# Kernel optimization log

Hardware: AMD Instinct MI355X
Metric: run time of the kernel (lower is better)

## Reference

```python
import jax, jax.numpy as jnp
import numpy as np

B, S1, S2 = 8, 2048, 2048
K1_DIM = K2_DIM = 512
PK1_DIM = PK2_DIM = 256
ATT_DIM = 512
DV = 512


def setup_inputs() -> dict:
    key = jax.random.key(0)
    ks = jax.random.split(key, 16)
    s = 0.02
    inp = {
        "k1": jax.random.normal(ks[0], (B, S1, K1_DIM), jnp.float32),
        "k2": jax.random.normal(ks[1], (B, S2, K2_DIM), jnp.float32),
        "preserved_k1": jax.random.normal(ks[2], (B, S1, PK1_DIM), jnp.float32),
        "preserved_k2": jax.random.normal(ks[3], (B, S2, PK2_DIM), jnp.float32),
        "v1": jax.random.normal(ks[4], (B, S1, DV), jnp.float32),
        "v2": jax.random.normal(ks[5], (B, S2, DV), jnp.float32),
        # Linear params stored as [in, out] (x @ W + b == torch Linear)
        "W_k1": jax.random.normal(ks[6], (K1_DIM, ATT_DIM), jnp.float32) * s,
        "b_k1": jnp.zeros((ATT_DIM,), jnp.float32),
        "W_k2": jax.random.normal(ks[7], (K2_DIM, ATT_DIM), jnp.float32) * s,
        "b_k2": jnp.zeros((ATT_DIM,), jnp.float32),
        "W_pk1": jax.random.normal(ks[8], (K1_DIM + PK1_DIM, ATT_DIM), jnp.float32) * s,
        "b_pk1": jnp.zeros((ATT_DIM,), jnp.float32),
        "W_pk2": jax.random.normal(ks[9], (K2_DIM + PK2_DIM, ATT_DIM), jnp.float32) * s,
        "b_pk2": jnp.zeros((ATT_DIM,), jnp.float32),
        # lengths in [S/2, S) so no softmax row is fully masked (original exits on NaN)
        "k1_lengths": jax.random.randint(ks[10], (B,), S1 // 2, S1, jnp.int32).astype(jnp.int64),
        "k2_lengths": jax.random.randint(ks[11], (B,), S2 // 2, S2, jnp.int32).astype(jnp.int64),
    }
    return inp


def _mask(k1_lengths, k2_lengths):
    # Faithful to the original loop: a position is masked iff EXACTLY ONE of
    # (row >= l1) / (col >= l2) holds (mask counter == 1, not >= 1).
    row_over = (jnp.arange(S1)[None, :, None] >= k1_lengths[:, None, None])  # [B,S1,1]
    col_over = (jnp.arange(S2)[None, None, :] >= k2_lengths[:, None, None])  # [B,1,S2]
    return (row_over.astype(jnp.int32) + col_over.astype(jnp.int32)) == 1  # [B,S1,S2]


def reference(k1, k2, preserved_k1, preserved_k2, v1, v2,
              W_k1, b_k1, W_k2, b_k2, W_pk1, b_pk1, W_pk2, b_pk2,
              k1_lengths, k2_lengths):
    pk1 = jnp.concatenate([k1, preserved_k1], axis=-1) @ W_pk1 + b_pk1  # [B,S1,A]
    pk2 = jnp.concatenate([k2, preserved_k2], axis=-1) @ W_pk2 + b_pk2  # [B,S2,A]
    k1p = k1 @ W_k1 + b_k1  # [B,S1,A]
    k2p = k2 @ W_k2 + b_k2  # [B,S2,A]

    score_1 = jnp.einsum("bsa,bta->bst", k1p, pk2)   # [B,S1,S2]
    score_2 = jnp.einsum("bsa,bta->bst", pk1, k2p)   # [B,S1,S2]

    mask = _mask(k1_lengths, k2_lengths)
    score_1 = jnp.where(mask, -jnp.inf, score_1)
    score_2 = jnp.where(mask, -jnp.inf, score_2)

    w1 = jax.nn.softmax(jnp.swapaxes(score_1, 1, 2), axis=-1)  # [B,S2,S1]
    w2 = jax.nn.softmax(score_2, axis=-1)                      # [B,S1,S2]

    o1 = jnp.einsum("bts,bsd->btd", w1, v1)  # [B,S2,DV]
    o2 = jnp.einsum("bst,btd->bsd", w2, v2)  # [B,S1,DV]
    # NOTE: original returns ragged per-sample slices of w1/w2; we return the
    # full padded weight matrices (slice w1[i,:l2,:l1], w2[i,:l1,:l2] to match).
    return (o1, o2, w1, w2)
```

## Files before the change

kernel.cpp:

```cpp
#include <hip/hip_runtime.h>

typedef _Float16 half8 __attribute__((ext_vector_type(8)));
typedef float    floatx4 __attribute__((ext_vector_type(4)));
typedef unsigned short u16;

constexpr int Bn  = 8;
constexpr int Sq  = 2048;
constexpr int KD  = 512;
constexpr int PKD = 256;
constexpr int AD  = 512;
constexpr int DV  = 512;

__device__ __forceinline__ void llds16(const void* g, void* l)
{
    __builtin_amdgcn_global_load_lds(
        (const __attribute__((address_space(1))) unsigned int*)g,
        (__attribute__((address_space(3))) unsigned int*)l, 16, 0, 0);
}

__global__ __launch_bounds__(256)
void transpose_cast_k(const float* __restrict__ in0, const float* __restrict__ in1,
                      _Float16* __restrict__ out0, _Float16* __restrict__ out1,
                      int inRows, int inCols, long long bsIn, long long bsOut,
                      int zsplit)
{
    __shared__ float t[32][33];
    const int bz = blockIdx.z;
    const bool sel = (bz >= zsplit);
    const int b = sel ? bz - zsplit : bz;
    const float* in = (sel ? in1 : in0) + (long long)b * bsIn;
    _Float16* out = (sel ? out1 : out0) + (long long)b * bsOut;
    const int tx = threadIdx.x & 31;
    const int ty = threadIdx.x >> 5;
    const int c0 = blockIdx.x * 32;
    const int r0 = blockIdx.y * 32;
#pragma unroll
    for (int i = 0; i < 4; ++i)
        t[ty + 8*i][tx] = in[(long long)(r0 + ty + 8*i) * inCols + c0 + tx];
    __syncthreads();
#pragma unroll
    for (int i = 0; i < 4; ++i)
        out[(long long)(c0 + ty + 8*i) * inRows + r0 + tx] = (_Float16)t[tx][ty + 8*i];
}

__global__ __launch_bounds__(256)
void wT_all_k(const float* __restrict__ Wk1, const float* __restrict__ Wk2,
              const float* __restrict__ Wpk1, const float* __restrict__ Wpk2,
              _Float16* __restrict__ Tk1, _Float16* __restrict__ Tk2,
              _Float16* __restrict__ Tpk1, _Float16* __restrict__ Tpk2)
{
    const int z = blockIdx.z;
    const float* W; _Float16* T; int Krows;
    if      (z == 0) { W = Wk1;  T = Tk1;  Krows = KD; }
    else if (z == 1) { W = Wk2;  T = Tk2;  Krows = KD; }
    else if (z == 2) { W = Wpk1; T = Tpk1; Krows = KD + PKD; }
    else             { W = Wpk2; T = Tpk2; Krows = KD + PKD; }
    const int r0 = blockIdx.y * 32;
    if (r0 >= Krows) return;
    const int c0 = blockIdx.x * 32;
    __shared__ float t[32][33];
    const int tx = threadIdx.x & 31;
    const int ty = threadIdx.x >> 5;
#pragma unroll
    for (int i = 0; i < 4; ++i)
        t[ty + 8*i][tx] = W[(long long)(r0 + ty + 8*i) * AD + c0 + tx];
    __syncthreads();
#pragma unroll
    for (int i = 0; i < 4; ++i)
        T[(long long)(c0 + ty + 8*i) * Krows + r0 + tx] = (_Float16)t[tx][ty + 8*i];
}

__global__ __launch_bounds__(256)
void cast_cat_k(const float* __restrict__ x0, const float* __restrict__ y0,
                _Float16* __restrict__ o0,
                const float* __restrict__ x1, const float* __restrict__ y1,
                _Float16* __restrict__ o1)
{
    const bool sel = (blockIdx.z != 0);
    const float* x = sel ? x1 : x0;
    const float* y = sel ? y1 : y0;
    _Float16* out = sel ? o1 : o0;
    const int idx = blockIdx.x * 256 + threadIdx.x;
    const int e   = idx * 8;
    const int r   = e / 768;
    const int c   = e % 768;
    const float* src = (c < 512) ? (x + (long long)r * 512 + c)
                                 : (y + (long long)r * 256 + (c - 512));
    const floatx4 f0 = *(const floatx4*)(src);
    const floatx4 f1 = *(const floatx4*)(src + 4);
    half8 h;
#pragma unroll
    for (int j = 0; j < 4; ++j) { h[j] = (_Float16)f0[j]; h[4 + j] = (_Float16)f1[j]; }
    *(half8*)(out + (long long)e) = h;
}

template<bool A_F32, bool OUT_F16>
__global__ __launch_bounds__(256, 2)
void gemm_k(const void* __restrict__ A1v, const void* __restrict__ A2v, int Ksplit,
            int lda1, int lda2, long long bsA,
            const _Float16* __restrict__ Bm, int ldb, long long bsB,
            void* __restrict__ Cv, int ldc, long long bsC,
            const float* __restrict__ bias, int K)
{
    __shared__ __align__(16) unsigned char AsRaw[A_F32 ? 16384 : 8192];
    __shared__ __align__(16) unsigned char BsRaw[8192];

    const int tid  = threadIdx.x;
    const int lane = tid & 63;
    const int wave = tid >> 6;
    const int wm   = (wave >> 1) * 64;
    const int wn   = (wave & 1) * 64;
    const int fr   = lane & 15;
    const int fq   = lane >> 4;

    const int tm = blockIdx.y, tn = blockIdx.x, bz = blockIdx.z;
    const long long aRowBase = (long long)tm * 128;
    const long long bRowBase = (long long)tn * 128;
    const _Float16* Bbase = Bm + (long long)bz * bsB;

    floatx4 acc[4][4];
#pragma unroll
    for (int i = 0; i < 4; ++i)
#pragma unroll
        for (int j = 0; j < 4; ++j) acc[i][j] = (floatx4)0.0f;

    for (int k0 = 0; k0 < K; k0 += 32) {
        __syncthreads();

        if (A_F32) {
            const float* A1 = (const float*)A1v + (long long)bz * bsA;
            const float* A2 = (const float*)A2v;
#pragma unroll
            for (int is = 0; is < 4; ++is) {
                const int r  = (tid >> 3) + is * 32;
                const int ch = (tid & 7) ^ (r & 7);
                const int kk = k0 + ch * 4;
                const float* src = (kk < Ksplit)
                    ? A1 + (aRowBase + r) * lda1 + kk
                    : A2 + (aRowBase + r) * lda2 + (kk - Ksplit);
                llds16(src, AsRaw + tid * 16 + is * 4096);
            }
        } else {
            const _Float16* A1 = (const _Float16*)A1v + (long long)bz * bsA;
#pragma unroll
            for (int is = 0; is < 2; ++is) {
                const int r  = (tid >> 2) + is * 64;
                const int ch = (tid & 3) ^ (r & 3);
                llds16(A1 + (aRowBase + r) * lda1 + k0 + ch * 8,
                       AsRaw + tid * 16 + is * 4096);
            }
        }
#pragma unroll
        for (int is = 0; is < 2; ++is) {
            const int r  = (tid >> 2) + is * 64;
            const int ch = (tid & 3) ^ (r & 3);
            llds16(Bbase + (bRowBase + r) * ldb + k0 + ch * 8,
                   BsRaw + tid * 16 + is * 4096);
        }

        __syncthreads();

        half8 af[4], bf[4];
        if (A_F32) {
            const float* As32 = (const float*)AsRaw;
#pragma unroll
            for (int i = 0; i < 4; ++i) {
                const int r  = wm + i * 16 + fr;
                const int c0 = ((2 * fq) ^ (r & 7)) * 4;
                const int c1 = ((2 * fq + 1) ^ (r & 7)) * 4;
                floatx4 f0 = *(const floatx4*)(As32 + r * 32 + c0);
                floatx4 f1 = *(const floatx4*)(As32 + r * 32 + c1);
                half8 h;
#pragma unroll
                for (int j = 0; j < 4; ++j) {
                    h[j]     = (_Float16)f0[j];
                    h[4 + j] = (_Float16)f1[j];
                }
                af[i] = h;
            }
        } else {
            const _Float16* As16 = (const _Float16*)AsRaw;
#pragma unroll
            for (int i = 0; i < 4; ++i) {
                const int r  = wm + i * 16 + fr;
                const int ch = fq ^ (r & 3);
                af[i] = *(const half8*)(As16 + r * 32 + ch * 8);
            }
        }
        {
            const _Float16* Bs16 = (const _Float16*)BsRaw;
#pragma unroll
            for (int j = 0; j < 4; ++j) {
                const int r  = wn + j * 16 + fr;
                const int ch = fq ^ (r & 3);
                bf[j] = *(const half8*)(Bs16 + r * 32 + ch * 8);
            }
        }
#pragma unroll
        for (int i = 0; i < 4; ++i)
#pragma unroll
            for (int j = 0; j < 4; ++j)
                acc[i][j] = __builtin_amdgcn_mfma_f32_16x16x32_f16(af[i], bf[j], acc[i][j], 0, 0, 0);
    }

    const int crow0 = tm * 128 + wm + fq * 4;
    const int ccol0 = tn * 128 + wn + fr;
    if (OUT_F16) {
        _Float16* C = (_Float16*)Cv + (long long)bz * bsC;
#pragma unroll
        for (int i = 0; i < 4; ++i)
#pragma unroll
            for (int j = 0; j < 4; ++j) {
                const int col = ccol0 + j * 16;
                const float bv = bias[col];
#pragma unroll
                for (int r = 0; r < 4; ++r)
                    C[(long long)(crow0 + i*16 + r) * ldc + col] = (_Float16)(acc[i][j][r] + bv);
            }
    } else {
        float* C = (float*)Cv + (long long)bz * bsC;
#pragma unroll
        for (int i = 0; i < 4; ++i)
#pragma unroll
            for (int j = 0; j < 4; ++j) {
                const int col = ccol0 + j * 16;
#pragma unroll
                for (int r = 0; r < 4; ++r)
                    C[(long long)(crow0 + i*16 + r) * ldc + col] = acc[i][j][r];
            }
    }
}

template<bool OUT16>
__global__ __launch_bounds__(512, 2)
void gemm256_k(const _Float16* __restrict__ A0, const _Float16* __restrict__ A1,
               const _Float16* __restrict__ B0, const _Float16* __restrict__ B1,
               void* __restrict__ C0v, void* __restrict__ C1v,
               long long bsA, int lda, long long bsB, int ldb,
               long long bsC, int ldc, int K, int zsplit)
{
    __shared__ __align__(16) _Float16 lds[65536];

    const int nwg  = 64 * gridDim.z;
    const int lin0 = (blockIdx.z * 8 + blockIdx.y) * 8 + blockIdx.x;
    const int cpx  = nwg >> 3;
    const int lin  = (lin0 & 7) * cpx + (lin0 >> 3);
    const int tn   = lin & 7;
    const int tm   = (lin >> 3) & 7;
    const int bz   = lin >> 6;

    const bool sel = (bz >= zsplit);
    const int  bzl = sel ? (bz - zsplit) : bz;
    const _Float16* Am = sel ? A1 : A0;
    const _Float16* Bm = sel ? B1 : B0;

    const int tid  = threadIdx.x;
    const int lane = tid & 63;
    const int wave = tid >> 6;
    const int wm   = (wave >> 2) * 128;
    const int wn   = (wave & 3) * 64;
    const int fr   = lane & 15;
    const int fq   = lane >> 4;

    const _Float16* Ab = Am + (long long)bzl * bsA + (long long)tm * 256 * lda;
    const _Float16* Bb = Bm + (long long)bzl * bsB + (long long)tn * 256 * ldb;

    const int sr = lane >> 3;
    const int ch = (lane & 7) ^ sr;
    const _Float16* srcA[2][2];
    const _Float16* srcB[2][2];
#pragma unroll
    for (int h = 0; h < 2; ++h)
#pragma unroll
        for (int l = 0; l < 2; ++l) {
            const int r = h * 128 + (wave * 2 + l) * 8 + sr;
            srcA[h][l] = Ab + (long long)r * lda + ch * 8;
            srcB[h][l] = Bb + (long long)r * ldb + ch * 8;
        }

    auto stageA = [&](int kt, int buf) {
#pragma unroll
        for (int h = 0; h < 2; ++h)
#pragma unroll
            for (int l = 0; l < 2; ++l)
                llds16(srcA[h][l] + kt * 64,
                       lds + buf * 32768 + h * 8192 + (wave * 2 + l) * 512 + lane * 8);
    };
    auto stageB = [&](int kt, int buf) {
#pragma unroll
        for (int h = 0; h < 2; ++h)
#pragma unroll
            for (int l = 0; l < 2; ++l)
                llds16(srcB[h][l] + kt * 64,
                       lds + buf * 32768 + 16384 + h * 8192 + (wave * 2 + l) * 512 + lane * 8);
    };

    auto rdA = [&](int buf, int im, int kk) -> half8 {
        const int row = wm + im * 16 + fr;
        const int c   = (kk * 4 + fq) ^ (row & 7);
        return *(const half8*)(lds + buf * 32768 + row * 64 + c * 8);
    };
    auto rdB = [&](int buf, int jn, int kk) -> half8 {
        const int row = wn + jn * 16 + fr;
        const int c   = (kk * 4 + fq) ^ (row & 7);
        return *(const half8*)(lds + buf * 32768 + 16384 + row * 64 + c * 8);
    };

    floatx4 acc[8][4];
#pragma unroll
    for (int i = 0; i < 8; ++i)
#pragma unroll
        for (int j = 0; j < 4; ++j) acc[i][j] = (floatx4)0.0f;

    const int KT = K >> 6;

    stageA(0, 0);
    stageB(0, 0);
    __syncthreads();

    for (int kt = 0; kt < KT; ++kt) {
        const int buf = kt & 1;
        half8 af[4][2], bf[2][2];
#pragma unroll
        for (int q = 0; q < 4; ++q) {
            const int nh = q >> 1;
            const int mh = (q == 1 || q == 2) ? 1 : 0;
            if (q == 0 || q == 2) {
#pragma unroll
                for (int j = 0; j < 2; ++j)
#pragma unroll
                    for (int kk = 0; kk < 2; ++kk)
                        bf[j][kk] = rdB(buf, nh * 2 + j, kk);
            }
            if (q != 2) {
#pragma unroll
                for (int i = 0; i < 4; ++i)
#pragma unroll
                    for (int kk = 0; kk < 2; ++kk)
                        af[i][kk] = rdA(buf, mh * 4 + i, kk);
            }
            if (kt + 1 < KT) {
                if (q == 0)      stageA(kt + 1, buf ^ 1);
                else if (q == 1) stageB(kt + 1, buf ^ 1);
            }
            __builtin_amdgcn_s_barrier();
            __builtin_amdgcn_s_setprio(1);
#pragma unroll
            for (int i = 0; i < 4; ++i)
#pragma unroll
                for (int j = 0; j < 2; ++j)
#pragma unroll
                    for (int kk = 0; kk < 2; ++kk)
                        acc[mh * 4 + i][nh * 2 + j] =
                            __builtin_amdgcn_mfma_f32_16x16x32_f16(
                                af[i][kk], bf[j][kk], acc[mh * 4 + i][nh * 2 + j], 0, 0, 0);
            __builtin_amdgcn_s_setprio(0);
            if (q < 3) __builtin_amdgcn_s_barrier();
        }
        __syncthreads();
    }

    const int crow0 = tm * 256 + wm + fq * 4;
    const int ccol0 = tn * 256 + wn + fr;
    if (OUT16) {
        _Float16* Cb = (_Float16*)(sel ? C1v : C0v) + (long long)bzl * bsC;
#pragma unroll
        for (int i = 0; i < 8; ++i)
#pragma unroll
            for (int j = 0; j < 4; ++j) {
                const long long base = (long long)(crow0 + i * 16) * ldc + ccol0 + j * 16;
#pragma unroll
                for (int r = 0; r < 4; ++r)
                    Cb[base + (long long)r * ldc] = (_Float16)acc[i][j][r];
            }
    } else {
        float* Cb = (float*)(sel ? C1v : C0v) + (long long)bzl * bsC;
#pragma unroll
        for (int i = 0; i < 8; ++i)
#pragma unroll
            for (int j = 0; j < 4; ++j) {
                const long long base = (long long)(crow0 + i * 16) * ldc + ccol0 + j * 16;
#pragma unroll
                for (int r = 0; r < 4; ++r)
                    Cb[base + (long long)r * ldc] = acc[i][j][r];
            }
    }
}

template<bool OUT_F16>
__global__ __launch_bounds__(512, 2)
void gemm256x128_k(const _Float16* __restrict__ A0, const _Float16* __restrict__ A1,
                   long long bsA, int lda,
                   const _Float16* __restrict__ B0, const _Float16* __restrict__ B1,
                   long long bsB, int ldb,
                   void* __restrict__ C0, void* __restrict__ C1,
                   long long bsC, int ldc,
                   const float* __restrict__ bias0, const float* __restrict__ bias1,
                   int K, int zsplit)
{
    __shared__ __align__(16) _Float16 lds[49152];

    const int gx   = gridDim.x, gy = gridDim.y;
    const int nwg  = gx * gy * gridDim.z;
    const int lin0 = (blockIdx.z * gy + blockIdx.y) * gx + blockIdx.x;
    const int cpx  = nwg >> 3;
    const int lin  = (lin0 & 7) * cpx + (lin0 >> 3);
    const int tn   = lin % gx;
    const int tmp2 = lin / gx;
    const int tm   = tmp2 % gy;
    const int bz   = tmp2 / gy;

    const bool sel = (bz >= zsplit);
    const int  bzl = sel ? (bz - zsplit) : bz;
    const _Float16* Am = sel ? A1 : A0;
    const _Float16* Bm = sel ? B1 : B0;

    const int tid  = threadIdx.x;
    const int lane = tid & 63;
    const int wave = tid >> 6;
    const int wm   = (wave >> 2) * 128;
    const int wn   = (wave & 3) * 32;
    const int fr   = lane & 15;
    const int fq   = lane >> 4;

    const _Float16* Ab = Am + (long long)bzl * bsA + (long long)tm * 256 * lda;
    const _Float16* Bb = Bm + (long long)bzl * bsB + (long long)tn * 128 * ldb;

    const int sr = lane >> 3;
    const int ch = (lane & 7) ^ sr;
    const _Float16* srcA[2][2];
    const _Float16* srcB[2];
#pragma unroll
    for (int h = 0; h < 2; ++h)
#pragma unroll
        for (int l = 0; l < 2; ++l)
            srcA[h][l] = Ab + (long long)(h * 128 + (wave * 2 + l) * 8 + sr) * lda + ch * 8;
#pragma unroll
    for (int l = 0; l < 2; ++l)
        srcB[l] = Bb + (long long)((wave * 2 + l) * 8 + sr) * ldb + ch * 8;

    auto stageA = [&](int kt, int buf) {
#pragma unroll
        for (int h = 0; h < 2; ++h)
#pragma unroll
            for (int l = 0; l < 2; ++l)
                llds16(srcA[h][l] + kt * 64,
                       lds + buf * 24576 + h * 8192 + (wave * 2 + l) * 512 + lane * 8);
    };
    auto stageB = [&](int kt, int buf) {
#pragma unroll
        for (int l = 0; l < 2; ++l)
            llds16(srcB[l] + kt * 64,
                   lds + buf * 24576 + 16384 + (wave * 2 + l) * 512 + lane * 8);
    };

    auto rdA = [&](int buf, int im, int kk) -> half8 {
        const int row = wm + im * 16 + fr;
        const int c   = (kk * 4 + fq) ^ (row & 7);
        return *(const half8*)(lds + buf * 24576 + row * 64 + c * 8);
    };
    auto rdB = [&](int buf, int jn, int kk) -> half8 {
        const int row = wn + jn * 16 + fr;
        const int c   = (kk * 4 + fq) ^ (row & 7);
        return *(const half8*)(lds + buf * 24576 + 16384 + row * 64 + c * 8);
    };

    floatx4 acc[8][2];
#pragma unroll
    for (int i = 0; i < 8; ++i)
#pragma unroll
        for (int j = 0; j < 2; ++j) acc[i][j] = (floatx4)0.0f;

    const int KT = K >> 6;

    stageA(0, 0);
    stageB(0, 0);
    __syncthreads();

    for (int kt = 0; kt < KT; ++kt) {
        const int buf = kt & 1;
        half8 afA[4][2], afB[4][2], bf0[2], bf1[2];

#pragma unroll
        for (int kk = 0; kk < 2; ++kk) bf0[kk] = rdB(buf, 0, kk);
#pragma unroll
        for (int i = 0; i < 4; ++i)
#pragma unroll
            for (int kk = 0; kk < 2; ++kk) afA[i][kk] = rdA(buf, i, kk);
        if (kt + 1 < KT) stageA(kt + 1, buf ^ 1);
        __builtin_amdgcn_s_barrier();
        __builtin_amdgcn_s_setprio(1);
#pragma unroll
        for (int i = 0; i < 4; ++i)
#pragma unroll
            for (int kk = 0; kk < 2; ++kk)
                acc[i][0] = __builtin_amdgcn_mfma_f32_16x16x32_f16(afA[i][kk], bf0[kk], acc[i][0], 0, 0, 0);
        __builtin_amdgcn_s_setprio(0);
        __builtin_amdgcn_s_barrier();

#pragma unroll
        for (int i = 0; i < 4; ++i)
#pragma unroll
            for (int kk = 0; kk < 2; ++kk) afB[i][kk] = rdA(buf, 4 + i, kk);
        if (kt + 1 < KT) stageB(kt + 1, buf ^ 1);
        __builtin_amdgcn_s_barrier();
        __builtin_amdgcn_s_setprio(1);
#pragma unroll
        for (int i = 0; i < 4; ++i)
#pragma unroll
            for (int kk = 0; kk < 2; ++kk)
                acc[4 + i][0] = __builtin_amdgcn_mfma_f32_16x16x32_f16(afB[i][kk], bf0[kk], acc[4 + i][0], 0, 0, 0);
        __builtin_amdgcn_s_setprio(0);
        __builtin_amdgcn_s_barrier();

#pragma unroll
        for (int kk = 0; kk < 2; ++kk) bf1[kk] = rdB(buf, 1, kk);
        __builtin_amdgcn_s_barrier();
        __builtin_amdgcn_s_setprio(1);
#pragma unroll
        for (int i = 0; i < 4; ++i)
#pragma unroll
            for (int kk = 0; kk < 2; ++kk)
                acc[4 + i][1] = __builtin_amdgcn_mfma_f32_16x16x32_f16(afB[i][kk], bf1[kk], acc[4 + i][1], 0, 0, 0);
        __builtin_amdgcn_s_setprio(0);
        __builtin_amdgcn_s_barrier();

        __builtin_amdgcn_s_setprio(1);
#pragma unroll
        for (int i = 0; i < 4; ++i)
#pragma unroll
            for (int kk = 0; kk < 2; ++kk)
                acc[i][1] = __builtin_amdgcn_mfma_f32_16x16x32_f16(afA[i][kk], bf1[kk], acc[i][1], 0, 0, 0);
        __builtin_amdgcn_s_setprio(0);

        __syncthreads();
    }

    const int crow0 = tm * 256 + wm + fq * 4;
    const int ccol0 = tn * 128 + wn + fr;
    if (OUT_F16) {
        const float* bias = sel ? bias1 : bias0;
        _Float16* C = (_Float16*)(sel ? C1 : C0) + (long long)bzl * bsC;
#pragma unroll
        for (int i = 0; i < 8; ++i)
#pragma unroll
            for (int j = 0; j < 2; ++j) {
                const int col = ccol0 + j * 16;
                const float bv = bias[col];
#pragma unroll
                for (int r = 0; r < 4; ++r)
                    C[(long long)(crow0 + i * 16 + r) * ldc + col] = (_Float16)(acc[i][j][r] + bv);
            }
    } else {
        float* C = (float*)(sel ? C1 : C0) + (long long)bzl * bsC;
#pragma unroll
        for (int i = 0; i < 8; ++i)
#pragma unroll
            for (int j = 0; j < 2; ++j) {
                const int col = ccol0 + j * 16;
#pragma unroll
                for (int r = 0; r < 4; ++r)
                    C[(long long)(crow0 + i * 16 + r) * ldc + col] = acc[i][j][r];
            }
    }
}

__global__ __launch_bounds__(512, 2)
void gemm_proj_k(const _Float16* __restrict__ Acat1, const _Float16* __restrict__ Acat2,
                 const _Float16* __restrict__ B0, const _Float16* __restrict__ B1,
                 const _Float16* __restrict__ B2, const _Float16* __restrict__ B3,
                 _Float16* __restrict__ C0, _Float16* __restrict__ C1,
                 _Float16* __restrict__ C2, _Float16* __restrict__ C3,
                 const float* __restrict__ bias0, const float* __restrict__ bias1,
                 const float* __restrict__ bias2, const float* __restrict__ bias3,
                 int K0, int K1)
{
    __shared__ __align__(16) _Float16 lds[49152];

    const int nwg  = 4 * 64 * 4;
    const int lin0 = (blockIdx.z * 64 + blockIdx.y) * 4 + blockIdx.x;
    const int cpx  = nwg >> 3;
    const int lin  = (lin0 & 7) * cpx + (lin0 >> 3);
    const int tn   = lin & 3;
    const int tm   = (lin >> 2) & 63;
    const int pz   = lin >> 8;

    const _Float16* Am = (pz & 1) ? Acat2 : Acat1;
    const _Float16* Bm; _Float16* Cm; const float* bias; int K;
    if      (pz == 0) { Bm = B0; Cm = C0; bias = bias0; K = K0; }
    else if (pz == 1) { Bm = B1; Cm = C1; bias = bias1; K = K0; }
    else if (pz == 2) { Bm = B2; Cm = C2; bias = bias2; K = K1; }
    else              { Bm = B3; Cm = C3; bias = bias3; K = K1; }
    const int lda = KD + PKD;
    const int ldb = K;
    const int ldc = AD;

    const int tid  = threadIdx.x;
    const int lane = tid & 63;
    const int wave = tid >> 6;
    const int wm   = (wave >> 2) * 128;
    const int wn   = (wave & 3) * 32;
    const int fr   = lane & 15;
    const int fq   = lane >> 4;

    const _Float16* Ab = Am + (long long)tm * 256 * lda;
    const _Float16* Bb = Bm + (long long)tn * 128 * ldb;

    const int sr = lane >> 3;
    const int ch = (lane & 7) ^ sr;
    const _Float16* srcA[2][2];
    const _Float16* srcB[2];
#pragma unroll
    for (int h = 0; h < 2; ++h)
#pragma unroll
        for (int l = 0; l < 2; ++l)
            srcA[h][l] = Ab + (long long)(h * 128 + (wave * 2 + l) * 8 + sr) * lda + ch * 8;
#pragma unroll
    for (int l = 0; l < 2; ++l)
        srcB[l] = Bb + (long long)((wave * 2 + l) * 8 + sr) * ldb + ch * 8;

    auto stageA = [&](int kt, int buf) {
#pragma unroll
        for (int h = 0; h < 2; ++h)
#pragma unroll
            for (int l = 0; l < 2; ++l)
                llds16(srcA[h][l] + kt * 64,
                       lds + buf * 24576 + h * 8192 + (wave * 2 + l) * 512 + lane * 8);
    };
    auto stageB = [&](int kt, int buf) {
#pragma unroll
        for (int l = 0; l < 2; ++l)
            llds16(srcB[l] + kt * 64,
                   lds + buf * 24576 + 16384 + (wave * 2 + l) * 512 + lane * 8);
    };

    auto rdA = [&](int buf, int im, int kk) -> half8 {
        const int row = wm + im * 16 + fr;
        const int c   = (kk * 4 + fq) ^ (row & 7);
        return *(const half8*)(lds + buf * 24576 + row * 64 + c * 8);
    };
    auto rdB = [&](int buf, int jn, int kk) -> half8 {
        const int row = wn + jn * 16 + fr;
        const int c   = (kk * 4 + fq) ^ (row & 7);
        return *(const half8*)(lds + buf * 24576 + 16384 + row * 64 + c * 8);
    };

    floatx4 acc[8][2];
#pragma unroll
    for (int i = 0; i < 8; ++i)
#pragma unroll
        for (int j = 0; j < 2; ++j) acc[i][j] = (floatx4)0.0f;

    const int KT = K >> 6;

    stageA(0, 0);
    stageB(0, 0);
    __syncthreads();

    for (int kt = 0; kt < KT; ++kt) {
        const int buf = kt & 1;
        half8 afA[4][2], afB[4][2], bf0[2], bf1[2];

#pragma unroll
        for (int kk = 0; kk < 2; ++kk) bf0[kk] = rdB(buf, 0, kk);
#pragma unroll
        for (int i = 0; i < 4; ++i)
#pragma unroll
            for (int kk = 0; kk < 2; ++kk) afA[i][kk] = rdA(buf, i, kk);
        if (kt + 1 < KT) stageA(kt + 1, buf ^ 1);
        __builtin_amdgcn_s_barrier();
        __builtin_amdgcn_s_setprio(1);
#pragma unroll
        for (int i = 0; i < 4; ++i)
#pragma unroll
            for (int kk = 0; kk < 2; ++kk)
                acc[i][0] = __builtin_amdgcn_mfma_f32_16x16x32_f16(afA[i][kk], bf0[kk], acc[i][0], 0, 0, 0);
        __builtin_amdgcn_s_setprio(0);
        __builtin_amdgcn_s_barrier();

#pragma unroll
        for (int i = 0; i < 4; ++i)
#pragma unroll
            for (int kk = 0; kk < 2; ++kk) afB[i][kk] = rdA(buf, 4 + i, kk);
        if (kt + 1 < KT) stageB(kt + 1, buf ^ 1);
        __builtin_amdgcn_s_barrier();
        __builtin_amdgcn_s_setprio(1);
#pragma unroll
        for (int i = 0; i < 4; ++i)
#pragma unroll
            for (int kk = 0; kk < 2; ++kk)
                acc[4 + i][0] = __builtin_amdgcn_mfma_f32_16x16x32_f16(afB[i][kk], bf0[kk], acc[4 + i][0], 0, 0, 0);
        __builtin_amdgcn_s_setprio(0);
        __builtin_amdgcn_s_barrier();

#pragma unroll
        for (int kk = 0; kk < 2; ++kk) bf1[kk] = rdB(buf, 1, kk);
        __builtin_amdgcn_s_barrier();
        __builtin_amdgcn_s_setprio(1);
#pragma unroll
        for (int i = 0; i < 4; ++i)
#pragma unroll
            for (int kk = 0; kk < 2; ++kk)
                acc[4 + i][1] = __builtin_amdgcn_mfma_f32_16x16x32_f16(afB[i][kk], bf1[kk], acc[4 + i][1], 0, 0, 0);
        __builtin_amdgcn_s_setprio(0);
        __builtin_amdgcn_s_barrier();

        __builtin_amdgcn_s_setprio(1);
#pragma unroll
        for (int i = 0; i < 4; ++i)
#pragma unroll
            for (int kk = 0; kk < 2; ++kk)
                acc[i][1] = __builtin_amdgcn_mfma_f32_16x16x32_f16(afA[i][kk], bf1[kk], acc[i][1], 0, 0, 0);
        __builtin_amdgcn_s_setprio(0);

        __syncthreads();
    }

    const int crow0 = tm * 256 + wm + fq * 4;
    const int ccol0 = tn * 128 + wn + fr;
#pragma unroll
    for (int i = 0; i < 8; ++i)
#pragma unroll
        for (int j = 0; j < 2; ++j) {
            const int col = ccol0 + j * 16;
            const float bv = bias[col];
#pragma unroll
            for (int r = 0; r < 4; ++r)
                Cm[(long long)(crow0 + i * 16 + r) * ldc + col] = (_Float16)(acc[i][j][r] + bv);
        }
}

__device__ __forceinline__ int load_len(const int* __restrict__ p, int b)
{
    return (p[1] == 0) ? p[2 * b] : p[b];
}

template<bool F16IN>
__global__ __launch_bounds__(256)
void softmax_mask_k(float* __restrict__ w1p, float* __restrict__ w2p,
                    _Float16* __restrict__ wh1, _Float16* __restrict__ wh2,
                    const int* __restrict__ len1, const int* __restrict__ len2)
{
    const int z = blockIdx.z;
    float* w = z ? w2p : w1p;
    _Float16* wh = z ? wh2 : wh1;
    const int* lenR = z ? len1 : len2;
    const int* lenC = z ? len2 : len1;

    const int b = blockIdx.y;
    const int r = blockIdx.x;
    const long long rowOff = ((long long)b * Sq + r) * (long long)Sq;
    float* row = w + rowOff;
    const int lr = load_len(lenR, b);
    const int lc = load_len(lenC, b);
    const bool rover = (r >= lr);
    const int tid  = threadIdx.x;
    const int lane = tid & 63;
    const int wave = tid >> 6;

    float v[8];
    if (F16IN) {
        const half8 hv = *(const half8*)(wh + rowOff + tid * 8);
#pragma unroll
        for (int j = 0; j < 8; ++j) v[j] = (float)hv[j];
    } else {
        const floatx4 x0 = *(const floatx4*)(row + tid * 8);
        const floatx4 x1 = *(const floatx4*)(row + tid * 8 + 4);
#pragma unroll
        for (int j = 0; j < 4; ++j) { v[j] = x0[j]; v[4 + j] = x1[j]; }
    }

    float m = -3.0e38f;
#pragma unroll
    for (int j = 0; j < 8; ++j) {
        const int c = tid * 8 + j;
        if (rover != (c >= lc)) v[j] = -__builtin_inff();
        m = fmaxf(m, v[j]);
    }
#pragma unroll
    for (int off = 32; off > 0; off >>= 1) m = fmaxf(m, __shfl_xor(m, off, 64));
    __shared__ float redm[4], reds[4];
    if (lane == 0) redm[wave] = m;
    __syncthreads();
    m = fmaxf(fmaxf(redm[0], redm[1]), fmaxf(redm[2], redm[3]));

    float s = 0.f;
#pragma unroll
    for (int j = 0; j < 8; ++j) { v[j] = __expf(v[j] - m); s += v[j]; }
#pragma unroll
    for (int off = 32; off > 0; off >>= 1) s += __shfl_xor(s, off, 64);
    if (lane == 0) reds[wave] = s;
    __syncthreads();
    s = reds[0] + reds[1] + reds[2] + reds[3];
    const float inv = 1.0f / s;

    floatx4 x0, x1;
#pragma unroll
    for (int j = 0; j < 4; ++j) { x0[j] = v[j] * inv; x1[j] = v[4 + j] * inv; }
    *(floatx4*)(row + tid * 8)     = x0;
    *(floatx4*)(row + tid * 8 + 4) = x1;
    if (F16IN || wh != nullptr) {
        half8 h;
#pragma unroll
        for (int j = 0; j < 4; ++j) { h[j] = (_Float16)x0[j]; h[4 + j] = (_Float16)x1[j]; }
        *(half8*)(wh + rowOff + tid * 8) = h;
    }
}

extern "C" void kernel_launch(void* const* d_in, const int* in_sizes, int n_in,
                              void* d_out, int out_size, void* d_ws, size_t ws_size,
                              hipStream_t stream)
{
    (void)in_sizes; (void)n_in; (void)out_size;
    const float* k1    = (const float*)d_in[0];
    const float* k2    = (const float*)d_in[1];
    const float* pk1in = (const float*)d_in[2];
    const float* pk2in = (const float*)d_in[3];
    const float* v1    = (const float*)d_in[4];
    const float* v2    = (const float*)d_in[5];
    const float* W_k1  = (const float*)d_in[6];
    const float* b_k1  = (const float*)d_in[7];
    const float* W_k2  = (const float*)d_in[8];
    const float* b_k2  = (const float*)d_in[9];
    const float* W_pk1 = (const float*)d_in[10];
    const float* b_pk1 = (const float*)d_in[11];
    const float* W_pk2 = (const float*)d_in[12];
    const float* b_pk2 = (const float*)d_in[13];
    const int* len1 = (const int*)d_in[14];
    const int* len2 = (const int*)d_in[15];

    float* out = (float*)d_out;
    float* o1 = out;
    float* o2 = o1 + (long long)Bn * Sq * DV;
    float* w1 = o2 + (long long)Bn * Sq * DV;
    float* w2 = w1 + (long long)Bn * Sq * Sq;

    _Float16* k1p = (_Float16*)o1;
    _Float16* k2p = k1p + (long long)Bn * Sq * AD;
    _Float16* pk1 = (_Float16*)o2;
    _Float16* pk2 = pk1 + (long long)Bn * Sq * AD;
    _Float16* cat1 = pk2 + (long long)Bn * Sq * AD;
    _Float16* cat2 = cat1 + (long long)Bn * Sq * (KD + PKD);

    _Float16* vT1   = (_Float16*)d_ws;
    _Float16* vT2   = vT1 + (long long)Bn * DV * Sq;
    _Float16* WTk1  = vT2 + (long long)Bn * DV * Sq;
    _Float16* WTk2  = WTk1 + AD * KD;
    _Float16* WTpk1 = WTk2 + AD * KD;
    _Float16* WTpk2 = WTpk1 + AD * (KD + PKD);

    const unsigned long long fixedHalves =
        2ull * Bn * DV * Sq + 2ull * AD * KD + 2ull * AD * (KD + PKD);
    _Float16* w1h = (_Float16*)d_ws + fixedHalves;
    _Float16* w2h = w1h + (long long)Bn * Sq * Sq;
    const bool fast =
        ws_size >= (fixedHalves + 2ull * Bn * Sq * Sq) * sizeof(_Float16);

    wT_all_k<<<dim3(AD/32, (KD+PKD)/32, 4), 256, 0, stream>>>(
        W_k1, W_k2, W_pk1, W_pk2, WTk1, WTk2, WTpk1, WTpk2);
    transpose_cast_k<<<dim3(DV/32, Sq/32, 2*Bn), 256, 0, stream>>>(
        v1, v2, vT1, vT2, Sq, DV, (long long)Sq*DV, (long long)Sq*DV, Bn);
    cast_cat_k<<<dim3((Bn*Sq*(KD+PKD))/(256*8), 1, 2), 256, 0, stream>>>(
        k1, pk1in, cat1, k2, pk2in, cat2);

    gemm_proj_k<<<dim3(AD/128, (Bn*Sq)/256, 4), 512, 0, stream>>>(
        cat1, cat2,
        WTk1, WTk2, WTpk1, WTpk2,
        k1p, k2p, pk1, pk2,
        b_k1, b_k2, b_pk1, b_pk2,
        KD, KD + PKD);

    if (fast) {
        gemm256_k<true><<<dim3(Sq/256, Sq/256, 2*Bn), 512, 0, stream>>>(
            pk2, pk1, k1p, k2p, w1h, w2h,
            (long long)Sq*AD, AD, (long long)Sq*AD, AD,
            (long long)Sq*Sq, Sq, AD, Bn);
    } else {
        gemm256_k<false><<<dim3(Sq/256, Sq/256, 2*Bn), 512, 0, stream>>>(
            pk2, pk1, k1p, k2p, w1, w2,
            (long long)Sq*AD, AD, (long long)Sq*AD, AD,
            (long long)Sq*Sq, Sq, AD, Bn);
    }

    if (fast) {
        softmax_mask_k<true><<<dim3(Sq, Bn, 2), 256, 0, stream>>>(
            w1, w2, w1h, w2h, len1, len2);
    } else {
        softmax_mask_k<false><<<dim3(Sq, Bn, 2), 256, 0, stream>>>(
            w1, w2, nullptr, nullptr, len1, len2);
    }

    if (fast) {
        gemm256x128_k<false><<<dim3(DV/128, Sq/256, 2*Bn), 512, 0, stream>>>(
            w1h, w2h, (long long)Sq*Sq, Sq,
            vT1, vT2, (long long)DV*Sq, Sq,
            o1, o2, (long long)Sq*DV, DV,
            nullptr, nullptr, Sq, Bn);
    } else {
        const dim3 gOut(DV/128, Sq/128, Bn);
        gemm_k<true, false><<<gOut, 256, 0, stream>>>(
            w1, w1, Sq, Sq, Sq, (long long)Sq*Sq,
            vT1, Sq, (long long)DV*Sq,
            o1, DV, (long long)Sq*DV, nullptr, Sq);
        gemm_k<true, false><<<gOut, 256, 0, stream>>>(
            w2, w2, Sq, Sq, Sq, (long long)Sq*Sq,
            vT2, Sq, (long long)DV*Sq,
            o2, DV, (long long)Sq*DV, nullptr, Sq);
    }
}
```

Baseline: 792.1 us.

## Triple-buffer LDS in 256x128 GEMMs with prefetch distance two

Grows the LDS staging area from two to three buffers in the two 256x128 GEMM kernels, so global-to-LDS loads for tile kt+2 are issued while tile kt is computed. The per-iteration __syncthreads is replaced by a partial vmcnt wait plus a raw s_barrier, so loads stay in flight across iterations. This aims to hide global load latency, at the cost of 144KB of LDS per block, which may limit occupancy to one block per CU despite launch_bounds(512,2). The hard-coded vmcnt(6) assumes a fixed number of loads per stage.

```diff
diff --git a/kernel.cpp b/kernel.cpp
--- a/kernel.cpp
+++ b/kernel.cpp
@@ -398,7 +398,7 @@
                    const float* __restrict__ bias0, const float* __restrict__ bias1,
                    int K, int zsplit)
 {
-    __shared__ __align__(16) _Float16 lds[49152];
+    __shared__ __align__(16) _Float16 lds[73728];
 
     const int gx   = gridDim.x, gy = gridDim.y;
     const int nwg  = gx * gy * gridDim.z;
@@ -473,21 +473,29 @@
 
     const int KT = K >> 6;
 
-    stageA(0, 0);
-    stageB(0, 0);
-    __syncthreads();
-
+    stageA(0, 0); stageB(0, 0);
+    if (KT > 1) {
+        stageA(1, 1); stageB(1, 1);
+        asm volatile("s_waitcnt vmcnt(6)" ::: "memory");
+    } else {
+        asm volatile("s_waitcnt vmcnt(0)" ::: "memory");
+    }
+    __builtin_amdgcn_sched_barrier(0);
+    __builtin_amdgcn_s_barrier();
+    __builtin_amdgcn_sched_barrier(0);
+
+    int bufR = 0, bufP = 2;
     for (int kt = 0; kt < KT; ++kt) {
-        const int buf = kt & 1;
         half8 afA[4][2], afB[4][2], bf0[2], bf1[2];
-
-#pragma unroll
-        for (int kk = 0; kk < 2; ++kk) bf0[kk] = rdB(buf, 0, kk);
-#pragma unroll
-        for (int i = 0; i < 4; ++i)
-#pragma unroll
-            for (int kk = 0; kk < 2; ++kk) afA[i][kk] = rdA(buf, i, kk);
-        if (kt + 1 < KT) stageA(kt + 1, buf ^ 1);
+        const bool pf = (kt + 2 < KT);
+
+#pragma unroll
+        for (int kk = 0; kk < 2; ++kk) bf0[kk] = rdB(bufR, 0, kk);
+#pragma unroll
+        for (int i = 0; i < 4; ++i)
+#pragma unroll
+            for (int kk = 0; kk < 2; ++kk) afA[i][kk] = rdA(bufR, i, kk);
+        if (pf) stageA(kt + 2, bufP);
         __builtin_amdgcn_s_barrier();
         __builtin_amdgcn_s_setprio(1);
 #pragma unroll
@@ -501,8 +509,8 @@
 #pragma unroll
         for (int i = 0; i < 4; ++i)
 #pragma unroll
-            for (int kk = 0; kk < 2; ++kk) afB[i][kk] = rdA(buf, 4 + i, kk);
-        if (kt + 1 < KT) stageB(kt + 1, buf ^ 1);
+            for (int kk = 0; kk < 2; ++kk) afB[i][kk] = rdA(bufR, 4 + i, kk);
+        if (pf) stageB(kt + 2, bufP);
         __builtin_amdgcn_s_barrier();
         __builtin_amdgcn_s_setprio(1);
 #pragma unroll
@@ -514,7 +522,7 @@
         __builtin_amdgcn_s_barrier();
 
 #pragma unroll
-        for (int kk = 0; kk < 2; ++kk) bf1[kk] = rdB(buf, 1, kk);
+        for (int kk = 0; kk < 2; ++kk) bf1[kk] = rdB(bufR, 1, kk);
         __builtin_amdgcn_s_barrier();
         __builtin_amdgcn_s_setprio(1);
 #pragma unroll
@@ -533,7 +541,15 @@
                 acc[i][1] = __builtin_amdgcn_mfma_f32_16x16x32_f16(afA[i][kk], bf1[kk], acc[i][1], 0, 0, 0);
         __builtin_amdgcn_s_setprio(0);
 
-        __syncthreads();
+        if (kt + 1 < KT) {
+            if (pf) asm volatile("s_waitcnt vmcnt(6)" ::: "memory");
+            else    asm volatile("s_waitcnt vmcnt(0)" ::: "memory");
+            __builtin_amdgcn_sched_barrier(0);
+            __builtin_amdgcn_s_barrier();
+            __builtin_amdgcn_sched_barrier(0);
+        }
+        bufR = (bufR == 2) ? 0 : bufR + 1;
+        bufP = (bufP == 2) ? 0 : bufP + 1;
     }
 
     const int crow0 = tm * 256 + wm + fq * 4;
@@ -575,7 +591,7 @@
                  const float* __restrict__ bias2, const float* __restrict__ bias3,
                  int K0, int K1)
 {
-    __shared__ __align__(16) _Float16 lds[49152];
+    __shared__ __align__(16) _Float16 lds[73728];
 
     const int nwg  = 4 * 64 * 4;
     const int lin0 = (blockIdx.z * 64 + blockIdx.y) * 4 + blockIdx.x;
@@ -653,21 +669,29 @@
 
     const int KT = K >> 6;
 
-    stageA(0, 0);
-    stageB(0, 0);
-    __syncthreads();
-
+    stageA(0, 0); stageB(0, 0);
+    if (KT > 1) {
+        stageA(1, 1); stageB(1, 1);
+        asm volatile("s_waitcnt vmcnt(6)" ::: "memory");
+    } else {
+        asm volatile("s_waitcnt vmcnt(0)" ::: "memory");
+    }
+    __builtin_amdgcn_sched_barrier(0);
+    __builtin_amdgcn_s_barrier();
+    __builtin_amdgcn_sched_barrier(0);
+
+    int bufR = 0, bufP = 2;
     for (int kt = 0; kt < KT; ++kt) {
-        const int buf = kt & 1;
         half8 afA[4][2], afB[4][2], bf0[2], bf1[2];
-
-#pragma unroll
-        for (int kk = 0; kk < 2; ++kk) bf0[kk] = rdB(buf, 0, kk);
-#pragma unroll
-        for (int i = 0; i < 4; ++i)
-#pragma unroll
-            for (int kk = 0; kk < 2; ++kk) afA[i][kk] = rdA(buf, i, kk);
-        if (kt + 1 < KT) stageA(kt + 1, buf ^ 1);
+        const bool pf = (kt + 2 < KT);
+
+#pragma unroll
+        for (int kk = 0; kk < 2; ++kk) bf0[kk] = rdB(bufR, 0, kk);
+#pragma unroll
+        for (int i = 0; i < 4; ++i)
+#pragma unroll
+            for (int kk = 0; kk < 2; ++kk) afA[i][kk] = rdA(bufR, i, kk);
+        if (pf) stageA(kt + 2, bufP);
         __builtin_amdgcn_s_barrier();
         __builtin_amdgcn_s_setprio(1);
 #pragma unroll
@@ -681,8 +705,8 @@
 #pragma unroll
         for (int i = 0; i < 4; ++i)
 #pragma unroll
-            for (int kk = 0; kk < 2; ++kk) afB[i][kk] = rdA(buf, 4 + i, kk);
-        if (kt + 1 < KT) stageB(kt + 1, buf ^ 1);
+            for (int kk = 0; kk < 2; ++kk) afB[i][kk] = rdA(bufR, 4 + i, kk);
+        if (pf) stageB(kt + 2, bufP);
         __builtin_amdgcn_s_barrier();
         __builtin_amdgcn_s_setprio(1);
 #pragma unroll
@@ -694,7 +718,7 @@
         __builtin_amdgcn_s_barrier();
 
 #pragma unroll
-        for (int kk = 0; kk < 2; ++kk) bf1[kk] = rdB(buf, 1, kk);
+        for (int kk = 0; kk < 2; ++kk) bf1[kk] = rdB(bufR, 1, kk);
         __builtin_amdgcn_s_barrier();
         __builtin_amdgcn_s_setprio(1);
 #pragma unroll
@@ -713,7 +737,15 @@
                 acc[i][1] = __builtin_amdgcn_mfma_f32_16x16x32_f16(afA[i][kk], bf1[kk], acc[i][1], 0, 0, 0);
         __builtin_amdgcn_s_setprio(0);
 
-        __syncthreads();
+        if (kt + 1 < KT) {
+            if (pf) asm volatile("s_waitcnt vmcnt(6)" ::: "memory");
+            else    asm volatile("s_waitcnt vmcnt(0)" ::: "memory");
+            __builtin_amdgcn_sched_barrier(0);
+            __builtin_amdgcn_s_barrier();
+            __builtin_amdgcn_sched_barrier(0);
+        }
+        bufR = (bufR == 2) ? 0 : bufR + 1;
+        bufP = (bufP == 2) ? 0 : bufP + 1;
     }
 
     const int crow0 = tm * 256 + wm + fq * 4;
```

New measurement: 767.8 us. -3.1%, faster.
